# Performance work log

Hardware: AMD Instinct MI355X
Metric: run time of the kernel (lower is better)

Reference implementation:

```python
import jax, jax.numpy as jnp
import numpy as np

N_NODES = 50000
N_EDGES = 800000
DIM = 128
LN_EPS = 1e-5


def _gcn_conv(x, src, dst, W, b, n_nodes):
    h = x @ W  # [N, D]
    loop = jnp.arange(n_nodes, dtype=src.dtype)
    src_f = jnp.concatenate([src, loop])
    dst_f = jnp.concatenate([dst, loop])
    deg = jax.ops.segment_sum(jnp.ones_like(dst_f, dtype=h.dtype), dst_f,
                              num_segments=n_nodes)  # in-degree incl. self-loop (>=1)
    dinv = jax.lax.rsqrt(deg)
    norm = dinv[src_f] * dinv[dst_f]  # [E+N]
    msg = norm[:, None] * h[src_f]  # gather + scale
    out = jax.ops.segment_sum(msg, dst_f, num_segments=n_nodes)
    return out + b


def _layer_norm(h, w, b):
    mu = jnp.mean(h, axis=-1, keepdims=True)
    var = jnp.mean(jnp.square(h - mu), axis=-1, keepdims=True)
    return (h - mu) * jax.lax.rsqrt(var + LN_EPS) * w + b


def setup_inputs() -> dict:
    key = jax.random.key(0)
    ks = jax.random.split(key, 8)
    x = jax.random.normal(ks[0], (N_NODES, DIM), dtype=jnp.float32)
    edge_index = jax.random.randint(ks[1], (2, N_EDGES), 0, N_NODES, dtype=jnp.int64)
    s = 1.0 / np.sqrt(DIM)
    W0 = jax.random.uniform(ks[2], (DIM, DIM), jnp.float32, -s, s)
    b0 = jnp.zeros((DIM,), jnp.float32)
    W1 = jax.random.uniform(ks[3], (DIM, DIM), jnp.float32, -s, s)
    b1 = jnp.zeros((DIM,), jnp.float32)
    ln0_w = jnp.ones((DIM,), jnp.float32)
    ln0_b = jnp.zeros((DIM,), jnp.float32)
    ln1_w = jnp.ones((DIM,), jnp.float32)
    ln1_b = jnp.zeros((DIM,), jnp.float32)
    return {"x": x, "edge_index": edge_index, "W0": W0, "b0": b0, "W1": W1,
            "b1": b1, "ln0_w": ln0_w, "ln0_b": ln0_b, "ln1_w": ln1_w, "ln1_b": ln1_b}


def reference(x, edge_index, W0, b0, W1, b1, ln0_w, ln0_b, ln1_w, ln1_b):
    src, dst = edge_index[0], edge_index[1]
    n = x.shape[0]
    # layer 0 (dropout is identity in eval mode)
    h = _gcn_conv(x, src, dst, W0, b0, n)
    h = jax.nn.relu(_layer_norm(h, ln0_w, ln0_b)) + x
    # layer 1
    h2 = _gcn_conv(h, src, dst, W1, b1, n)
    h2 = jax.nn.relu(_layer_norm(h2, ln1_w, ln1_b)) + h
    return h2
```

## Files before the change

kernel.cpp:

```cpp
#include <hip/hip_runtime.h>
#include <hip/hip_bf16.h>

#define NDIM 128
#define NNODES 50000
#define CAP 64
#define SWZ(b) ((b) ^ ((((b) >> 8) & 7) << 4))
#define GEMM_GRID 782
#define BUILD_GRID 242

typedef short bf16x8 __attribute__((ext_vector_type(8)));
typedef float f32x4 __attribute__((ext_vector_type(4)));

__device__ __forceinline__ unsigned short f2bf(float f) {
    unsigned u = __builtin_bit_cast(unsigned, f);
    unsigned r = (u + 0x7FFF + ((u >> 16) & 1)) >> 16;
    return (unsigned short)r;
}
__device__ __forceinline__ float bf2f(unsigned short u) {
    return __builtin_bit_cast(float, (unsigned)u << 16);
}

__device__ __forceinline__ void gl_lds16(const void* g, void* l) {
    __builtin_amdgcn_global_load_lds(
        (const __attribute__((address_space(1))) unsigned int*)g,
        (__attribute__((address_space(3))) unsigned int*)l, 16, 0, 0);
}

__global__ __launch_bounds__(256) void k_prep(const float* __restrict__ W0,
                                              const float* __restrict__ W1,
                                              unsigned short* __restrict__ Ws0,
                                              unsigned short* __restrict__ Ws1) {
    int t = blockIdx.x * 256 + threadIdx.x;
    const float* W = (t >> 14) ? W1 : W0;
    unsigned short* Wd = (t >> 14) ? Ws1 : Ws0;
    int e = t & 16383;
    int k = e >> 7, c = e & 127;
    int byteb = c * 256 + k * 2;
    Wd[SWZ(byteb) >> 1] = f2bf(W[k * NDIM + c]);
}

__global__ __launch_bounds__(256) void k_mega(const float* __restrict__ X,
                                              const unsigned short* __restrict__ Wsw,
                                              unsigned short* __restrict__ Hb,
                                              const int* __restrict__ src,
                                              const int* __restrict__ dst,
                                              int* __restrict__ cnt,
                                              int* __restrict__ bucket,
                                              int E, int n) {
    __shared__ char sW[32768];
    if (blockIdx.x >= GEMM_GRID) {
        int e0 = (blockIdx.x - GEMM_GRID) * 256 + threadIdx.x;
        for (int e = e0; e < E; e += BUILD_GRID * 256) {
            int d = dst[e];
            int p = atomicAdd(&cnt[d], 1);
            if (p < CAP)
                __builtin_nontemporal_store(src[e], &bucket[(long)d * CAP + p]);
        }
        return;
    }
    const int wave = threadIdx.x >> 6, lane = threadIdx.x & 63;
    {
        const char* g = (const char*)Wsw;
#pragma unroll
        for (int i = 0; i < 8; i++) {
            int off = (i * 4 + wave) * 1024 + lane * 16;
            gl_lds16(g + off, sW + off);
        }
    }
    const int r16 = lane & 15, hi = lane >> 4;
    const int nodeb = blockIdx.x * 64 + wave * 16;
    int arow = nodeb + r16; if (arow > n - 1) arow = n - 1;

    bf16x8 a[4];
    const float* xp = X + (size_t)arow * NDIM + hi * 8;
#pragma unroll
    for (int kc = 0; kc < 4; kc++) {
        float4 f0 = *(const float4*)(xp + kc * 32);
        float4 f1 = *(const float4*)(xp + kc * 32 + 4);
        bf16x8 v;
        v[0] = f2bf(f0.x); v[1] = f2bf(f0.y); v[2] = f2bf(f0.z); v[3] = f2bf(f0.w);
        v[4] = f2bf(f1.x); v[5] = f2bf(f1.y); v[6] = f2bf(f1.z); v[7] = f2bf(f1.w);
        a[kc] = v;
    }
    __syncthreads();

#pragma unroll
    for (int ct = 0; ct < 8; ct++) {
        f32x4 acc = {0.f, 0.f, 0.f, 0.f};
#pragma unroll
        for (int kc = 0; kc < 4; kc++) {
            int bb = (ct * 16 + r16) * 256 + kc * 64 + hi * 16;
            bf16x8 bw = *(const bf16x8*)(sW + SWZ(bb));
            acc = __builtin_amdgcn_mfma_f32_16x16x32_bf16(a[kc], bw, acc, 0, 0, 0);
        }
#pragma unroll
        for (int r = 0; r < 4; r++) {
            int row = nodeb + hi * 4 + r;
            if (row < n)
                Hb[(size_t)row * NDIM + ct * 16 + r16] = f2bf(acc[r]);
        }
    }
}

__global__ __launch_bounds__(256) void k_scale(unsigned short* __restrict__ hb,
                                               const int* __restrict__ cnt,
                                               float* __restrict__ dinv) {
    const int tid = threadIdx.x;
    const int l16 = tid & 15;
    const int row = blockIdx.x * 16 + (tid >> 4);
    const float dv = rsqrtf((float)cnt[row] + 1.0f);
    if (l16 == 0) dinv[row] = dv;
    unsigned short* p = hb + (size_t)row * NDIM + l16 * 8;
    bf16x8 v = *(const bf16x8*)p;
    bf16x8 o;
#pragma unroll
    for (int t = 0; t < 8; t++)
        o[t] = (short)f2bf(bf2f((unsigned short)v[t]) * dv);
    *(bf16x8*)p = o;
}

__global__ __launch_bounds__(256) void k_gemm(const float* __restrict__ X,
                                              const unsigned short* __restrict__ Wsw,
                                              const float* __restrict__ dinv,
                                              unsigned short* __restrict__ Hb,
                                              int n) {
    __shared__ char sW[32768];
    const int wave = threadIdx.x >> 6, lane = threadIdx.x & 63;
    {
        const char* g = (const char*)Wsw;
#pragma unroll
        for (int i = 0; i < 8; i++) {
            int off = (i * 4 + wave) * 1024 + lane * 16;
            gl_lds16(g + off, sW + off);
        }
    }
    const int r16 = lane & 15, hi = lane >> 4;
    const int nodeb = blockIdx.x * 64 + wave * 16;
    int arow = nodeb + r16; if (arow > n - 1) arow = n - 1;

    bf16x8 a[4];
    const float* xp = X + (size_t)arow * NDIM + hi * 8;
#pragma unroll
    for (int kc = 0; kc < 4; kc++) {
        float4 f0 = *(const float4*)(xp + kc * 32);
        float4 f1 = *(const float4*)(xp + kc * 32 + 4);
        bf16x8 v;
        v[0] = f2bf(f0.x); v[1] = f2bf(f0.y); v[2] = f2bf(f0.z); v[3] = f2bf(f0.w);
        v[4] = f2bf(f1.x); v[5] = f2bf(f1.y); v[6] = f2bf(f1.z); v[7] = f2bf(f1.w);
        a[kc] = v;
    }
    float dr[4];
#pragma unroll
    for (int r = 0; r < 4; r++) {
        int row = nodeb + hi * 4 + r;
        dr[r] = dinv[row < n ? row : n - 1];
    }
    __syncthreads();

#pragma unroll
    for (int ct = 0; ct < 8; ct++) {
        f32x4 acc = {0.f, 0.f, 0.f, 0.f};
#pragma unroll
        for (int kc = 0; kc < 4; kc++) {
            int bb = (ct * 16 + r16) * 256 + kc * 64 + hi * 16;
            bf16x8 bw = *(const bf16x8*)(sW + SWZ(bb));
            acc = __builtin_amdgcn_mfma_f32_16x16x32_bf16(a[kc], bw, acc, 0, 0, 0);
        }
#pragma unroll
        for (int r = 0; r < 4; r++) {
            int row = nodeb + hi * 4 + r;
            if (row < n)
                Hb[(size_t)row * NDIM + ct * 16 + r16] = f2bf(acc[r] * dr[r]);
        }
    }
}

__global__ __launch_bounds__(256) void k_agg(const unsigned short* __restrict__ hb,
                                             const float* __restrict__ xres,
                                             const int* __restrict__ bucket,
                                             const int* __restrict__ cnt,
                                             const float* __restrict__ dinv,
                                             const float* __restrict__ bias,
                                             const float* __restrict__ lnw,
                                             const float* __restrict__ lnb,
                                             float* __restrict__ out) {
    const int tid = threadIdx.x;
    const int l16 = tid & 15;
    const int node = blockIdx.x * 16 + (tid >> 4);
    const int d0 = l16 * 8;

    const float dv = dinv[node];
    int c = cnt[node]; if (c > CAP) c = CAP;

    float acc[8];
    {
        bf16x8 sv = *(const bf16x8*)(hb + (size_t)node * NDIM + d0);
#pragma unroll
        for (int t = 0; t < 8; t++) acc[t] = bf2f((unsigned short)sv[t]);
    }

    const int* bk = bucket + (size_t)node * CAP;
    int j = 0;
    for (; j + 8 <= c; j += 8) {
        bf16x8 r0 = *(const bf16x8*)(hb + (size_t)bk[j    ] * NDIM + d0);
        bf16x8 r1 = *(const bf16x8*)(hb + (size_t)bk[j + 1] * NDIM + d0);
        bf16x8 r2 = *(const bf16x8*)(hb + (size_t)bk[j + 2] * NDIM + d0);
        bf16x8 r3 = *(const bf16x8*)(hb + (size_t)bk[j + 3] * NDIM + d0);
        bf16x8 r4 = *(const bf16x8*)(hb + (size_t)bk[j + 4] * NDIM + d0);
        bf16x8 r5 = *(const bf16x8*)(hb + (size_t)bk[j + 5] * NDIM + d0);
        bf16x8 r6 = *(const bf16x8*)(hb + (size_t)bk[j + 6] * NDIM + d0);
        bf16x8 r7 = *(const bf16x8*)(hb + (size_t)bk[j + 7] * NDIM + d0);
#pragma unroll
        for (int t = 0; t < 8; t++)
            acc[t] += ((bf2f((unsigned short)r0[t]) + bf2f((unsigned short)r1[t]))
                     + (bf2f((unsigned short)r2[t]) + bf2f((unsigned short)r3[t])))
                    + ((bf2f((unsigned short)r4[t]) + bf2f((unsigned short)r5[t]))
                     + (bf2f((unsigned short)r6[t]) + bf2f((unsigned short)r7[t])));
    }
    for (; j + 4 <= c; j += 4) {
        bf16x8 r0 = *(const bf16x8*)(hb + (size_t)bk[j    ] * NDIM + d0);
        bf16x8 r1 = *(const bf16x8*)(hb + (size_t)bk[j + 1] * NDIM + d0);
        bf16x8 r2 = *(const bf16x8*)(hb + (size_t)bk[j + 2] * NDIM + d0);
        bf16x8 r3 = *(const bf16x8*)(hb + (size_t)bk[j + 3] * NDIM + d0);
#pragma unroll
        for (int t = 0; t < 8; t++)
            acc[t] += (bf2f((unsigned short)r0[t]) + bf2f((unsigned short)r1[t]))
                    + (bf2f((unsigned short)r2[t]) + bf2f((unsigned short)r3[t]));
    }
    for (; j < c; j++) {
        bf16x8 r = *(const bf16x8*)(hb + (size_t)bk[j] * NDIM + d0);
#pragma unroll
        for (int t = 0; t < 8; t++) acc[t] += bf2f((unsigned short)r[t]);
    }

    float v[8];
    float4 bb0 = *(const float4*)(bias + d0);
    float4 bb1 = *(const float4*)(bias + d0 + 4);
    v[0] = fmaf(dv, acc[0], bb0.x); v[1] = fmaf(dv, acc[1], bb0.y);
    v[2] = fmaf(dv, acc[2], bb0.z); v[3] = fmaf(dv, acc[3], bb0.w);
    v[4] = fmaf(dv, acc[4], bb1.x); v[5] = fmaf(dv, acc[5], bb1.y);
    v[6] = fmaf(dv, acc[6], bb1.z); v[7] = fmaf(dv, acc[7], bb1.w);

    float s = 0.f;
#pragma unroll
    for (int t = 0; t < 8; t++) s += v[t];
#pragma unroll
    for (int o = 1; o < 16; o <<= 1) s += __shfl_xor(s, o);
    const float mu = s * (1.0f / 128.0f);

    float e[8], q = 0.f;
#pragma unroll
    for (int t = 0; t < 8; t++) { e[t] = v[t] - mu; q += e[t] * e[t]; }
#pragma unroll
    for (int o = 1; o < 16; o <<= 1) q += __shfl_xor(q, o);
    const float rinv = rsqrtf(q * (1.0f / 128.0f) + 1e-5f);

    float4 w0 = *(const float4*)(lnw + d0), w1 = *(const float4*)(lnw + d0 + 4);
    float4 lb0 = *(const float4*)(lnb + d0), lb1 = *(const float4*)(lnb + d0 + 4);
    float4 x0 = *(const float4*)(xres + (size_t)node * NDIM + d0);
    float4 x1 = *(const float4*)(xres + (size_t)node * NDIM + d0 + 4);

    float4 o0, o1;
    o0.x = fmaxf(fmaf(e[0] * rinv, w0.x, lb0.x), 0.f) + x0.x;
    o0.y = fmaxf(fmaf(e[1] * rinv, w0.y, lb0.y), 0.f) + x0.y;
    o0.z = fmaxf(fmaf(e[2] * rinv, w0.z, lb0.z), 0.f) + x0.z;
    o0.w = fmaxf(fmaf(e[3] * rinv, w0.w, lb0.w), 0.f) + x0.w;
    o1.x = fmaxf(fmaf(e[4] * rinv, w1.x, lb1.x), 0.f) + x1.x;
    o1.y = fmaxf(fmaf(e[5] * rinv, w1.y, lb1.y), 0.f) + x1.y;
    o1.z = fmaxf(fmaf(e[6] * rinv, w1.z, lb1.z), 0.f) + x1.z;
    o1.w = fmaxf(fmaf(e[7] * rinv, w1.w, lb1.w), 0.f) + x1.w;
    *(float4*)(out + (size_t)node * NDIM + d0) = o0;
    *(float4*)(out + (size_t)node * NDIM + d0 + 4) = o1;
}

extern "C" void kernel_launch(void* const* d_in, const int* in_sizes, int n_in,
                              void* d_out, int out_size, void* d_ws, size_t ws_size,
                              hipStream_t stream) {
    const float* x    = (const float*)d_in[0];
    const int*   ei   = (const int*)d_in[1];
    const float* W0   = (const float*)d_in[2];
    const float* b0   = (const float*)d_in[3];
    const float* W1   = (const float*)d_in[4];
    const float* b1   = (const float*)d_in[5];
    const float* ln0w = (const float*)d_in[6];
    const float* ln0b = (const float*)d_in[7];
    const float* ln1w = (const float*)d_in[8];
    const float* ln1b = (const float*)d_in[9];
    float* out = (float*)d_out;

    const int E = in_sizes[1] / 2;
    const int* src = ei;
    const int* dst = ei + E;

    char* ws = (char*)d_ws;
    size_t o = 0;
    int*   cnt    = (int*)(ws + o);                  o += (size_t)50048 * 4;
    float* dinv   = (float*)(ws + o);                o += (size_t)50048 * 4;
    int*   bucket = (int*)(ws + o);                  o += (size_t)NNODES * CAP * 4;
    unsigned short* hb = (unsigned short*)(ws + o);  o += (size_t)NNODES * NDIM * 2;
    float* xmid   = (float*)(ws + o);                o += (size_t)NNODES * NDIM * 4;
    unsigned short* Ws0 = (unsigned short*)(ws + o); o += (size_t)NDIM * NDIM * 2;
    unsigned short* Ws1 = (unsigned short*)(ws + o); o += (size_t)NDIM * NDIM * 2;

    hipMemsetAsync(cnt, 0, NNODES * sizeof(int), stream);
    k_prep<<<128, 256, 0, stream>>>(W0, W1, Ws0, Ws1);

    k_mega<<<GEMM_GRID + BUILD_GRID, 256, 0, stream>>>(x, Ws0, hb, src, dst,
                                                       cnt, bucket, E, NNODES);
    k_scale<<<NNODES / 16, 256, 0, stream>>>(hb, cnt, dinv);
    k_agg<<<NNODES / 16, 256, 0, stream>>>(hb, x, bucket, cnt, dinv, b0,
                                           ln0w, ln0b, xmid);
    k_gemm<<<GEMM_GRID, 256, 0, stream>>>(xmid, Ws1, dinv, hb, NNODES);
    k_agg<<<NNODES / 16, 256, 0, stream>>>(hb, xmid, bucket, cnt, dinv, b1,
                                           ln1w, ln1b, out);
}
```

Baseline: 220.7 us.

## Fuse layer-0 aggregation and LayerNorm into layer-1 GEMM, use 16-bit buckets

Merges the first aggregation/LayerNorm/residual kernel with the second GEMM so the normalized features are packed to bf16 in LDS and fed directly into MFMA, avoiding a global reload of xmid. Bucket neighbor indices are stored as 16-bit values to halve index traffic. The CSR-bucket build now partitions destination nodes into 8 ranges by block index so atomics on cnt stay localized, at the cost of every build block scanning all edges. The fused kernel has fewer blocks and more LDS, reducing parallelism for the gather phase.

```diff
diff --git a/kernel.cpp b/kernel.cpp
--- a/kernel.cpp
+++ b/kernel.cpp
@@ -4,6 +4,7 @@
 #define NDIM 128
 #define NNODES 50000
 #define CAP 64
+#define NSH 6250
 #define SWZ(b) ((b) ^ ((((b) >> 8) & 7) << 4))
 #define GEMM_GRID 782
 #define BUILD_GRID 242
@@ -19,7 +20,6 @@
 __device__ __forceinline__ float bf2f(unsigned short u) {
     return __builtin_bit_cast(float, (unsigned)u << 16);
 }
-
 __device__ __forceinline__ void gl_lds16(const void* g, void* l) {
     __builtin_amdgcn_global_load_lds(
         (const __attribute__((address_space(1))) unsigned int*)g,
@@ -45,16 +45,23 @@
                                               const int* __restrict__ src,
                                               const int* __restrict__ dst,
                                               int* __restrict__ cnt,
-                                              int* __restrict__ bucket,
+                                              unsigned short* __restrict__ bucket,
                                               int E, int n) {
     __shared__ char sW[32768];
     if (blockIdx.x >= GEMM_GRID) {
-        int e0 = (blockIdx.x - GEMM_GRID) * 256 + threadIdx.x;
-        for (int e = e0; e < E; e += BUILD_GRID * 256) {
+        const int rr = blockIdx.x & 7;
+        const int o  = (rr + 2) & 7;
+        const int b  = blockIdx.x - GEMM_GRID;
+        const int li = (b - o) >> 3;
+        const int nb = ((BUILD_GRID - 1 - o) >> 3) + 1;
+        const unsigned lo = (unsigned)(rr * NSH);
+        const int stride = nb * 256;
+        for (int e = li * 256 + (int)threadIdx.x; e < E; e += stride) {
             int d = dst[e];
-            int p = atomicAdd(&cnt[d], 1);
-            if (p < CAP)
-                __builtin_nontemporal_store(src[e], &bucket[(long)d * CAP + p]);
+            if ((unsigned)d - lo < (unsigned)NSH) {
+                int p = atomicAdd(&cnt[d], 1);
+                if (p < CAP) bucket[(size_t)d * CAP + p] = (unsigned short)src[e];
+            }
         }
         return;
     }
@@ -119,65 +126,165 @@
     *(bf16x8*)p = o;
 }
 
-__global__ __launch_bounds__(256) void k_gemm(const float* __restrict__ X,
-                                              const unsigned short* __restrict__ Wsw,
-                                              const float* __restrict__ dinv,
-                                              unsigned short* __restrict__ Hb,
-                                              int n) {
-    __shared__ char sW[32768];
+__global__ __launch_bounds__(256) void k_fgemm(const unsigned short* __restrict__ hb0,
+                                               const float* __restrict__ xres,
+                                               const unsigned short* __restrict__ bkt,
+                                               const int* __restrict__ cnt,
+                                               const float* __restrict__ dinv,
+                                               const float* __restrict__ bias,
+                                               const float* __restrict__ lnw,
+                                               const float* __restrict__ lnb,
+                                               const unsigned short* __restrict__ Wsw,
+                                               float* __restrict__ xmid,
+                                               unsigned short* __restrict__ hb1,
+                                               int n) {
+    __shared__ char sMem[49152];
     const int wave = threadIdx.x >> 6, lane = threadIdx.x & 63;
     {
         const char* g = (const char*)Wsw;
 #pragma unroll
         for (int i = 0; i < 8; i++) {
             int off = (i * 4 + wave) * 1024 + lane * 16;
-            gl_lds16(g + off, sW + off);
-        }
-    }
+            gl_lds16(g + off, sMem + off);
+        }
+    }
+    const int tid = threadIdx.x;
+    const int l16 = tid & 15;
+    const int grp = tid >> 4;
+    const int d0 = l16 * 8;
+    const int nodeb = blockIdx.x * 64;
+
+#pragma unroll 1
+    for (int k = 0; k < 4; k++) {
+        const int ln = grp * 4 + k;
+        const int node = nodeb + ln;
+        if (node < n) {
+            const float dv = dinv[node];
+            int c = cnt[node]; if (c > CAP) c = CAP;
+            float acc[8];
+            {
+                bf16x8 sv = *(const bf16x8*)(hb0 + (size_t)node * NDIM + d0);
+#pragma unroll
+                for (int t = 0; t < 8; t++) acc[t] = bf2f((unsigned short)sv[t]);
+            }
+            const unsigned short* bk = bkt + (size_t)node * CAP;
+            int j = 0;
+            for (; j + 8 <= c; j += 8) {
+                bf16x8 r0 = *(const bf16x8*)(hb0 + (size_t)bk[j    ] * NDIM + d0);
+                bf16x8 r1 = *(const bf16x8*)(hb0 + (size_t)bk[j + 1] * NDIM + d0);
+                bf16x8 r2 = *(const bf16x8*)(hb0 + (size_t)bk[j + 2] * NDIM + d0);
+                bf16x8 r3 = *(const bf16x8*)(hb0 + (size_t)bk[j + 3] * NDIM + d0);
+                bf16x8 r4 = *(const bf16x8*)(hb0 + (size_t)bk[j + 4] * NDIM + d0);
+                bf16x8 r5 = *(const bf16x8*)(hb0 + (size_t)bk[j + 5] * NDIM + d0);
+                bf16x8 r6 = *(const bf16x8*)(hb0 + (size_t)bk[j + 6] * NDIM + d0);
+                bf16x8 r7 = *(const bf16x8*)(hb0 + (size_t)bk[j + 7] * NDIM + d0);
+#pragma unroll
+                for (int t = 0; t < 8; t++)
+                    acc[t] += ((bf2f((unsigned short)r0[t]) + bf2f((unsigned short)r1[t]))
+                             + (bf2f((unsigned short)r2[t]) + bf2f((unsigned short)r3[t])))
+                            + ((bf2f((unsigned short)r4[t]) + bf2f((unsigned short)r5[t]))
+                             + (bf2f((unsigned short)r6[t]) + bf2f((unsigned short)r7[t])));
+            }
+            for (; j + 4 <= c; j += 4) {
+                bf16x8 r0 = *(const bf16x8*)(hb0 + (size_t)bk[j    ] * NDIM + d0);
+                bf16x8 r1 = *(const bf16x8*)(hb0 + (size_t)bk[j + 1] * NDIM + d0);
+                bf16x8 r2 = *(const bf16x8*)(hb0 + (size_t)bk[j + 2] * NDIM + d0);
+                bf16x8 r3 = *(const bf16x8*)(hb0 + (size_t)bk[j + 3] * NDIM + d0);
+#pragma unroll
+                for (int t = 0; t < 8; t++)
+                    acc[t] += (bf2f((unsigned short)r0[t]) + bf2f((unsigned short)r1[t]))
+                            + (bf2f((unsigned short)r2[t]) + bf2f((unsigned short)r3[t]));
+            }
+            for (; j < c; j++) {
+                bf16x8 r = *(const bf16x8*)(hb0 + (size_t)bk[j] * NDIM + d0);
+#pragma unroll
+                for (int t = 0; t < 8; t++) acc[t] += bf2f((unsigned short)r[t]);
+            }
+
+            float v[8];
+            float4 bb0 = *(const float4*)(bias + d0);
+            float4 bb1 = *(const float4*)(bias + d0 + 4);
+            v[0] = fmaf(dv, acc[0], bb0.x); v[1] = fmaf(dv, acc[1], bb0.y);
+            v[2] = fmaf(dv, acc[2], bb0.z); v[3] = fmaf(dv, acc[3], bb0.w);
+            v[4] = fmaf(dv, acc[4], bb1.x); v[5] = fmaf(dv, acc[5], bb1.y);
+            v[6] = fmaf(dv, acc[6], bb1.z); v[7] = fmaf(dv, acc[7], bb1.w);
+
+            float s = 0.f;
+#pragma unroll
+            for (int t = 0; t < 8; t++) s += v[t];
+#pragma unroll
+            for (int o = 1; o < 16; o <<= 1) s += __shfl_xor(s, o);
+            const float mu = s * (1.0f / 128.0f);
+            float e[8], q = 0.f;
+#pragma unroll
+            for (int t = 0; t < 8; t++) { e[t] = v[t] - mu; q += e[t] * e[t]; }
+#pragma unroll
+            for (int o = 1; o < 16; o <<= 1) q += __shfl_xor(q, o);
+            const float rinv = rsqrtf(q * (1.0f / 128.0f) + 1e-5f);
+
+            float4 w0 = *(const float4*)(lnw + d0), w1 = *(const float4*)(lnw + d0 + 4);
+            float4 lb0 = *(const float4*)(lnb + d0), lb1 = *(const float4*)(lnb + d0 + 4);
+            float4 x0 = *(const float4*)(xres + (size_t)node * NDIM + d0);
+            float4 x1 = *(const float4*)(xres + (size_t)node * NDIM + d0 + 4);
+
+            float4 o0, o1;
+            o0.x = fmaxf(fmaf(e[0] * rinv, w0.x, lb0.x), 0.f) + x0.x;
+            o0.y = fmaxf(fmaf(e[1] * rinv, w0.y, lb0.y), 0.f) + x0.y;
+            o0.z = fmaxf(fmaf(e[2] * rinv, w0.z, lb0.z), 0.f) + x0.z;
+            o0.w = fmaxf(fmaf(e[3] * rinv, w0.w, lb0.w), 0.f) + x0.w;
+            o1.x = fmaxf(fmaf(e[4] * rinv, w1.x, lb1.x), 0.f) + x1.x;
+            o1.y = fmaxf(fmaf(e[5] * rinv, w1.y, lb1.y), 0.f) + x1.y;
+            o1.z = fmaxf(fmaf(e[6] * rinv, w1.z, lb1.z), 0.f) + x1.z;
+            o1.w = fmaxf(fmaf(e[7] * rinv, w1.w, lb1.w), 0.f) + x1.w;
+            *(float4*)(xmid + (size_t)node * NDIM + d0) = o0;
+            *(float4*)(xmid + (size_t)node * NDIM + d0 + 4) = o1;
+
+            bf16x8 pk;
+            pk[0] = (short)f2bf(o0.x); pk[1] = (short)f2bf(o0.y);
+            pk[2] = (short)f2bf(o0.z); pk[3] = (short)f2bf(o0.w);
+            pk[4] = (short)f2bf(o1.x); pk[5] = (short)f2bf(o1.y);
+            pk[6] = (short)f2bf(o1.z); pk[7] = (short)f2bf(o1.w);
+            int bb = ln * 256 + l16 * 16;
+            *(bf16x8*)(sMem + 32768 + SWZ(bb)) = pk;
+        }
+    }
+    __syncthreads();
+
     const int r16 = lane & 15, hi = lane >> 4;
-    const int nodeb = blockIdx.x * 64 + wave * 16;
-    int arow = nodeb + r16; if (arow > n - 1) arow = n - 1;
-
+    const int arow = wave * 16 + r16;
     bf16x8 a[4];
-    const float* xp = X + (size_t)arow * NDIM + hi * 8;
 #pragma unroll
     for (int kc = 0; kc < 4; kc++) {
-        float4 f0 = *(const float4*)(xp + kc * 32);
-        float4 f1 = *(const float4*)(xp + kc * 32 + 4);
-        bf16x8 v;
-        v[0] = f2bf(f0.x); v[1] = f2bf(f0.y); v[2] = f2bf(f0.z); v[3] = f2bf(f0.w);
-        v[4] = f2bf(f1.x); v[5] = f2bf(f1.y); v[6] = f2bf(f1.z); v[7] = f2bf(f1.w);
-        a[kc] = v;
+        int bb = arow * 256 + kc * 64 + hi * 16;
+        a[kc] = *(const bf16x8*)(sMem + 32768 + SWZ(bb));
     }
     float dr[4];
 #pragma unroll
     for (int r = 0; r < 4; r++) {
-        int row = nodeb + hi * 4 + r;
+        int row = nodeb + wave * 16 + hi * 4 + r;
         dr[r] = dinv[row < n ? row : n - 1];
     }
-    __syncthreads();
-
 #pragma unroll
     for (int ct = 0; ct < 8; ct++) {
         f32x4 acc = {0.f, 0.f, 0.f, 0.f};
 #pragma unroll
         for (int kc = 0; kc < 4; kc++) {
             int bb = (ct * 16 + r16) * 256 + kc * 64 + hi * 16;
-            bf16x8 bw = *(const bf16x8*)(sW + SWZ(bb));
+            bf16x8 bw = *(const bf16x8*)(sMem + SWZ(bb));
             acc = __builtin_amdgcn_mfma_f32_16x16x32_bf16(a[kc], bw, acc, 0, 0, 0);
         }
 #pragma unroll
         for (int r = 0; r < 4; r++) {
-            int row = nodeb + hi * 4 + r;
+            int row = nodeb + wave * 16 + hi * 4 + r;
             if (row < n)
-                Hb[(size_t)row * NDIM + ct * 16 + r16] = f2bf(acc[r] * dr[r]);
+                hb1[(size_t)row * NDIM + ct * 16 + r16] = f2bf(acc[r] * dr[r]);
         }
     }
 }
 
 __global__ __launch_bounds__(256) void k_agg(const unsigned short* __restrict__ hb,
                                              const float* __restrict__ xres,
-                                             const int* __restrict__ bucket,
+                                             const unsigned short* __restrict__ bkt,
                                              const int* __restrict__ cnt,
                                              const float* __restrict__ dinv,
                                              const float* __restrict__ bias,
@@ -198,8 +305,7 @@
 #pragma unroll
         for (int t = 0; t < 8; t++) acc[t] = bf2f((unsigned short)sv[t]);
     }
-
-    const int* bk = bucket + (size_t)node * CAP;
+    const unsigned short* bk = bkt + (size_t)node * CAP;
     int j = 0;
     for (; j + 8 <= c; j += 8) {
         bf16x8 r0 = *(const bf16x8*)(hb + (size_t)bk[j    ] * NDIM + d0);
@@ -294,23 +400,23 @@
 
     char* ws = (char*)d_ws;
     size_t o = 0;
-    int*   cnt    = (int*)(ws + o);                  o += (size_t)50048 * 4;
-    float* dinv   = (float*)(ws + o);                o += (size_t)50048 * 4;
-    int*   bucket = (int*)(ws + o);                  o += (size_t)NNODES * CAP * 4;
-    unsigned short* hb = (unsigned short*)(ws + o);  o += (size_t)NNODES * NDIM * 2;
-    float* xmid   = (float*)(ws + o);                o += (size_t)NNODES * NDIM * 4;
-    unsigned short* Ws0 = (unsigned short*)(ws + o); o += (size_t)NDIM * NDIM * 2;
-    unsigned short* Ws1 = (unsigned short*)(ws + o); o += (size_t)NDIM * NDIM * 2;
+    int*   cnt    = (int*)(ws + o);                   o += (size_t)50048 * 4;
+    float* dinv   = (float*)(ws + o);                 o += (size_t)50048 * 4;
+    unsigned short* bkt = (unsigned short*)(ws + o);  o += (size_t)NNODES * CAP * 2;
+    unsigned short* hb0 = (unsigned short*)(ws + o);  o += (size_t)NNODES * NDIM * 2;
+    unsigned short* hb1 = (unsigned short*)(ws + o);  o += (size_t)NNODES * NDIM * 2;
+    float* xmid   = (float*)(ws + o);                 o += (size_t)NNODES * NDIM * 4;
+    unsigned short* Ws0 = (unsigned short*)(ws + o);  o += (size_t)NDIM * NDIM * 2;
+    unsigned short* Ws1 = (unsigned short*)(ws + o);  o += (size_t)NDIM * NDIM * 2;
 
     hipMemsetAsync(cnt, 0, NNODES * sizeof(int), stream);
     k_prep<<<128, 256, 0, stream>>>(W0, W1, Ws0, Ws1);
 
-    k_mega<<<GEMM_GRID + BUILD_GRID, 256, 0, stream>>>(x, Ws0, hb, src, dst,
-                                                       cnt, bucket, E, NNODES);
-    k_scale<<<NNODES / 16, 256, 0, stream>>>(hb, cnt, dinv);
-    k_agg<<<NNODES / 16, 256, 0, stream>>>(hb, x, bucket, cnt, dinv, b0,
-                                           ln0w, ln0b, xmid);
-    k_gemm<<<GEMM_GRID, 256, 0, stream>>>(xmid, Ws1, dinv, hb, NNODES);
-    k_agg<<<NNODES / 16, 256, 0, stream>>>(hb, xmid, bucket, cnt, dinv, b1,
+    k_mega<<<GEMM_GRID + BUILD_GRID, 256, 0, stream>>>(x, Ws0, hb0, src, dst,
+                                                       cnt, bkt, E, NNODES);
+    k_scale<<<NNODES / 16, 256, 0, stream>>>(hb0, cnt, dinv);
+    k_fgemm<<<GEMM_GRID, 256, 0, stream>>>(hb0, x, bkt, cnt, dinv, b0,
+                                           ln0w, ln0b, Ws1, xmid, hb1, NNODES);
+    k_agg<<<NNODES / 16, 256, 0, stream>>>(hb1, xmid, bkt, cnt, dinv, b1,
                                            ln1w, ln1b, out);
 }
```

New measurement: 288.8 us. 1.31x slower.

## Shrink neighbor buckets to 16-bit indices and double rows per GEMM wave

Applied to the files above, without the earlier changes.

Neighbor bucket entries are stored as unsigned short instead of int, which halves the bucket table's footprint and the index traffic in both aggregation passes. The indices stay valid only because node ids are below 65536. The second-layer GEMM now has each wave compute two 16-row tiles that share every LDS weight load, so it launches half as many blocks and loads the weights into LDS half as often. Separate bf16 buffers are used for each layer's transformed features. The costs are a node-count limit of 65536 and higher register pressure in the GEMM.

```diff
diff --git a/kernel.cpp b/kernel.cpp
--- a/kernel.cpp
+++ b/kernel.cpp
@@ -6,6 +6,7 @@
 #define CAP 64
 #define SWZ(b) ((b) ^ ((((b) >> 8) & 7) << 4))
 #define GEMM_GRID 782
+#define GEMM1_GRID 391
 #define BUILD_GRID 242
 
 typedef short bf16x8 __attribute__((ext_vector_type(8)));
@@ -19,7 +20,6 @@
 __device__ __forceinline__ float bf2f(unsigned short u) {
     return __builtin_bit_cast(float, (unsigned)u << 16);
 }
-
 __device__ __forceinline__ void gl_lds16(const void* g, void* l) {
     __builtin_amdgcn_global_load_lds(
         (const __attribute__((address_space(1))) unsigned int*)g,
@@ -45,7 +45,7 @@
                                               const int* __restrict__ src,
                                               const int* __restrict__ dst,
                                               int* __restrict__ cnt,
-                                              int* __restrict__ bucket,
+                                              unsigned short* __restrict__ bucket,
                                               int E, int n) {
     __shared__ char sW[32768];
     if (blockIdx.x >= GEMM_GRID) {
@@ -54,7 +54,8 @@
             int d = dst[e];
             int p = atomicAdd(&cnt[d], 1);
             if (p < CAP)
-                __builtin_nontemporal_store(src[e], &bucket[(long)d * CAP + p]);
+                __builtin_nontemporal_store((unsigned short)src[e],
+                                            &bucket[(size_t)d * CAP + p]);
         }
         return;
     }
@@ -135,49 +136,59 @@
         }
     }
     const int r16 = lane & 15, hi = lane >> 4;
-    const int nodeb = blockIdx.x * 64 + wave * 16;
-    int arow = nodeb + r16; if (arow > n - 1) arow = n - 1;
-
-    bf16x8 a[4];
-    const float* xp = X + (size_t)arow * NDIM + hi * 8;
-#pragma unroll
-    for (int kc = 0; kc < 4; kc++) {
-        float4 f0 = *(const float4*)(xp + kc * 32);
-        float4 f1 = *(const float4*)(xp + kc * 32 + 4);
-        bf16x8 v;
-        v[0] = f2bf(f0.x); v[1] = f2bf(f0.y); v[2] = f2bf(f0.z); v[3] = f2bf(f0.w);
-        v[4] = f2bf(f1.x); v[5] = f2bf(f1.y); v[6] = f2bf(f1.z); v[7] = f2bf(f1.w);
-        a[kc] = v;
-    }
-    float dr[4];
-#pragma unroll
-    for (int r = 0; r < 4; r++) {
-        int row = nodeb + hi * 4 + r;
-        dr[r] = dinv[row < n ? row : n - 1];
-    }
+    const int base = blockIdx.x * 128 + wave * 32;
+
+    bf16x8 a[2][4];
+#pragma unroll
+    for (int t = 0; t < 2; t++) {
+        int arow = base + t * 16 + r16; if (arow > n - 1) arow = n - 1;
+        const float* xp = X + (size_t)arow * NDIM + hi * 8;
+#pragma unroll
+        for (int kc = 0; kc < 4; kc++) {
+            float4 f0 = *(const float4*)(xp + kc * 32);
+            float4 f1 = *(const float4*)(xp + kc * 32 + 4);
+            bf16x8 v;
+            v[0] = f2bf(f0.x); v[1] = f2bf(f0.y); v[2] = f2bf(f0.z); v[3] = f2bf(f0.w);
+            v[4] = f2bf(f1.x); v[5] = f2bf(f1.y); v[6] = f2bf(f1.z); v[7] = f2bf(f1.w);
+            a[t][kc] = v;
+        }
+    }
+    float dr[2][4];
+#pragma unroll
+    for (int t = 0; t < 2; t++)
+#pragma unroll
+        for (int r = 0; r < 4; r++) {
+            int row = base + t * 16 + hi * 4 + r;
+            dr[t][r] = dinv[row < n ? row : n - 1];
+        }
     __syncthreads();
 
 #pragma unroll
     for (int ct = 0; ct < 8; ct++) {
-        f32x4 acc = {0.f, 0.f, 0.f, 0.f};
+        f32x4 acc0 = {0.f, 0.f, 0.f, 0.f};
+        f32x4 acc1 = {0.f, 0.f, 0.f, 0.f};
 #pragma unroll
         for (int kc = 0; kc < 4; kc++) {
             int bb = (ct * 16 + r16) * 256 + kc * 64 + hi * 16;
             bf16x8 bw = *(const bf16x8*)(sW + SWZ(bb));
-            acc = __builtin_amdgcn_mfma_f32_16x16x32_bf16(a[kc], bw, acc, 0, 0, 0);
+            acc0 = __builtin_amdgcn_mfma_f32_16x16x32_bf16(a[0][kc], bw, acc0, 0, 0, 0);
+            acc1 = __builtin_amdgcn_mfma_f32_16x16x32_bf16(a[1][kc], bw, acc1, 0, 0, 0);
         }
 #pragma unroll
         for (int r = 0; r < 4; r++) {
-            int row = nodeb + hi * 4 + r;
-            if (row < n)
-                Hb[(size_t)row * NDIM + ct * 16 + r16] = f2bf(acc[r] * dr[r]);
+            int row0 = base + hi * 4 + r;
+            if (row0 < n)
+                Hb[(size_t)row0 * NDIM + ct * 16 + r16] = f2bf(acc0[r] * dr[0][r]);
+            int row1 = base + 16 + hi * 4 + r;
+            if (row1 < n)
+                Hb[(size_t)row1 * NDIM + ct * 16 + r16] = f2bf(acc1[r] * dr[1][r]);
         }
     }
 }
 
 __global__ __launch_bounds__(256) void k_agg(const unsigned short* __restrict__ hb,
                                              const float* __restrict__ xres,
-                                             const int* __restrict__ bucket,
+                                             const unsigned short* __restrict__ bkt,
                                              const int* __restrict__ cnt,
                                              const float* __restrict__ dinv,
                                              const float* __restrict__ bias,
@@ -198,8 +209,7 @@
 #pragma unroll
         for (int t = 0; t < 8; t++) acc[t] = bf2f((unsigned short)sv[t]);
     }
-
-    const int* bk = bucket + (size_t)node * CAP;
+    const unsigned short* bk = bkt + (size_t)node * CAP;
     int j = 0;
     for (; j + 8 <= c; j += 8) {
         bf16x8 r0 = *(const bf16x8*)(hb + (size_t)bk[j    ] * NDIM + d0);
@@ -294,23 +304,24 @@
 
     char* ws = (char*)d_ws;
     size_t o = 0;
-    int*   cnt    = (int*)(ws + o);                  o += (size_t)50048 * 4;
-    float* dinv   = (float*)(ws + o);                o += (size_t)50048 * 4;
-    int*   bucket = (int*)(ws + o);                  o += (size_t)NNODES * CAP * 4;
-    unsigned short* hb = (unsigned short*)(ws + o);  o += (size_t)NNODES * NDIM * 2;
-    float* xmid   = (float*)(ws + o);                o += (size_t)NNODES * NDIM * 4;
-    unsigned short* Ws0 = (unsigned short*)(ws + o); o += (size_t)NDIM * NDIM * 2;
-    unsigned short* Ws1 = (unsigned short*)(ws + o); o += (size_t)NDIM * NDIM * 2;
+    int*   cnt    = (int*)(ws + o);                   o += (size_t)50048 * 4;
+    float* dinv   = (float*)(ws + o);                 o += (size_t)50048 * 4;
+    unsigned short* bkt = (unsigned short*)(ws + o);  o += (size_t)NNODES * CAP * 2;
+    unsigned short* hb0 = (unsigned short*)(ws + o);  o += (size_t)NNODES * NDIM * 2;
+    unsigned short* hb1 = (unsigned short*)(ws + o);  o += (size_t)NNODES * NDIM * 2;
+    float* xmid   = (float*)(ws + o);                 o += (size_t)NNODES * NDIM * 4;
+    unsigned short* Ws0 = (unsigned short*)(ws + o);  o += (size_t)NDIM * NDIM * 2;
+    unsigned short* Ws1 = (unsigned short*)(ws + o);  o += (size_t)NDIM * NDIM * 2;
 
     hipMemsetAsync(cnt, 0, NNODES * sizeof(int), stream);
     k_prep<<<128, 256, 0, stream>>>(W0, W1, Ws0, Ws1);
 
-    k_mega<<<GEMM_GRID + BUILD_GRID, 256, 0, stream>>>(x, Ws0, hb, src, dst,
-                                                       cnt, bucket, E, NNODES);
-    k_scale<<<NNODES / 16, 256, 0, stream>>>(hb, cnt, dinv);
-    k_agg<<<NNODES / 16, 256, 0, stream>>>(hb, x, bucket, cnt, dinv, b0,
+    k_mega<<<GEMM_GRID + BUILD_GRID, 256, 0, stream>>>(x, Ws0, hb0, src, dst,
+                                                       cnt, bkt, E, NNODES);
+    k_scale<<<NNODES / 16, 256, 0, stream>>>(hb0, cnt, dinv);
+    k_agg<<<NNODES / 16, 256, 0, stream>>>(hb0, x, bkt, cnt, dinv, b0,
                                            ln0w, ln0b, xmid);
-    k_gemm<<<GEMM_GRID, 256, 0, stream>>>(xmid, Ws1, dinv, hb, NNODES);
-    k_agg<<<NNODES / 16, 256, 0, stream>>>(hb, xmid, bucket, cnt, dinv, b1,
+    k_gemm<<<GEMM1_GRID, 256, 0, stream>>>(xmid, Ws1, dinv, hb1, NNODES);
+    k_agg<<<NNODES / 16, 256, 0, stream>>>(hb1, xmid, bkt, cnt, dinv, b1,
                                            ln1w, ln1b, out);
 }
```

New measurement: 217.4 us. No clear change (-1.5%).
